# Kernel optimization log

Hardware: AMD Instinct MI355X
Metric: run time of the kernel (lower is better)

The kernel has to match this reference:

```python
import jax, jax.numpy as jnp
import numpy as np

N = 100000   # nodes
E = 1600000  # edges (before self-loops)
IN = 128     # in_num
H1, C1 = 8, 8    # gat1: 8 heads x 8 channels -> 64 concat
OUT = 32     # out_num (gat2: 1 head x 32)


def setup_inputs() -> dict:
    key = jax.random.key(0)
    ks = jax.random.split(key, 10)
    g = lambda k, shape, fan: (jax.random.normal(k, shape, jnp.float32) / np.sqrt(fan).astype(np.float32))
    return {
        "x": jax.random.normal(ks[0], (N, IN), jnp.float32),
        "edge_index": jax.random.randint(ks[1], (2, E), 0, N, dtype=jnp.int64),
        "W1": g(ks[2], (IN, H1 * C1), IN),
        "a_src1": g(ks[3], (H1, C1), C1),
        "a_dst1": g(ks[4], (H1, C1), C1),
        "b1": jnp.zeros((H1 * C1,), jnp.float32),
        "W2": g(ks[5], (H1 * C1, OUT), H1 * C1),
        "a_src2": g(ks[6], (1, OUT), OUT),
        "a_dst2": g(ks[7], (1, OUT), OUT),
        "b2": jnp.zeros((OUT,), jnp.float32),
    }


def _gat_layer(x, src, dst, W, a_src, a_dst, b, heads, ch):
    # PyG GATConv (concat=True, negative_slope=0.2). Dropout (p=0.6) is a
    # no-op in eval mode and omitted.
    n = x.shape[0]
    h = (x @ W).reshape(n, heads, ch)                        # [N,H,C]
    al_s = jnp.einsum('nhc,hc->nh', h, a_src)                # [N,H]
    al_d = jnp.einsum('nhc,hc->nh', h, a_dst)
    e = jax.nn.leaky_relu(al_s[src] + al_d[dst], negative_slope=0.2)  # [E,H]
    # segment softmax over incoming edges of each dst node
    m = jax.lax.stop_gradient(jax.ops.segment_max(e, dst, num_segments=n))
    ex = jnp.exp(e - m[dst])
    denom = jax.ops.segment_sum(ex, dst, num_segments=n)
    alpha = ex / denom[dst]                                  # [E,H]
    out = jax.ops.segment_sum(h[src] * alpha[:, :, None], dst, num_segments=n)
    return out.reshape(n, heads * ch) + b


def reference(x, edge_index, W1, a_src1, a_dst1, b1, W2, a_src2, a_dst2, b2):
    loop = jnp.arange(N, dtype=edge_index.dtype)
    src = jnp.concatenate([edge_index[0], loop])  # add_self_loops=True (PyG default)
    dst = jnp.concatenate([edge_index[1], loop])
    h = _gat_layer(x, src, dst, W1, a_src1, a_dst1, b1, H1, C1)   # [N,64]
    out = _gat_layer(h, src, dst, W2, a_src2, a_dst2, b2, 1, OUT)  # [N,OUT]
    return out
```

## Files before the change

### kernel.cpp

```cpp
#include <hip/hip_runtime.h>
#include <hip/hip_bf16.h>


#define SLAB  4096
#define NBUCK 512

typedef float v2f __attribute__((ext_vector_type(2)));

__device__ __forceinline__ float lrelu02(float x) { return x > 0.f ? x : 0.2f * x; }

__device__ __forceinline__ unsigned short f2bf(float v) {
    __hip_bfloat16 b = __float2bfloat16(v);
    return __builtin_bit_cast(unsigned short, b);
}

__device__ __forceinline__ void accum8(uint4 hv, float ex, v2f* acc) {
    v2f ex2 = {ex, ex};
#pragma unroll
    for (int q = 0; q < 4; ++q) {
        unsigned u = (&hv.x)[q];
        v2f h2 = {__uint_as_float(u << 16), __uint_as_float(u & 0xffff0000u)};
        acc[q] = __builtin_elementwise_fma(h2, ex2, acc[q]);
    }
}

__device__ __forceinline__ v2f shfl_xor_v2(v2f v, int mask) {
    v2f r;
    r.x = __shfl_xor(v.x, mask, 64);
    r.y = __shfl_xor(v.y, mask, 64);
    return r;
}

__device__ __forceinline__ void scatter_body(char* smem, int vbid,
                                             const int* __restrict__ ei,
                                             int e_real, int e_total, unsigned M,
                                             int* __restrict__ bcur_pad,
                                             int2* __restrict__ pairs) {
    int*  cnt   = (int*)smem;
    int*  loff  = cnt + 512;
    int*  lcur  = loff + 512;
    int*  gbase = lcur + 512;
    int*  ssrc  = gbase + 512;
    int*  sdst  = ssrc + 2048;
    unsigned short* bb = (unsigned short*)(sdst + 2048);

    const int t = threadIdx.x;
    const int base = vbid * 2048;
    cnt[t] = 0; cnt[t + 256] = 0;
    __syncthreads();

    int rs[8], rd[8], rb[8];
#pragma unroll
    for (int k = 0; k < 8; ++k) {
        int i = base + k * 256 + t;
        bool val = i < e_total;
        int s = 0, d = 0;
        if (val) {
            if (i < e_real) { s = ei[i]; d = ei[e_real + i]; }
            else            { s = d = i - e_real; }
        }
        int b = val ? (int)__umulhi((unsigned)d, M) : -1;
        rs[k] = s; rd[k] = d; rb[k] = b;
        if (val) atomicAdd(&cnt[b], 1);
    }
    __syncthreads();

    loff[t] = cnt[t]; loff[t + 256] = cnt[t + 256];
    __syncthreads();
    for (int off = 1; off < 512; off <<= 1) {
        int v0 = (t >= off) ? loff[t - off] : 0;
        int v1 = (t + 256 >= off) ? loff[t + 256 - off] : 0;
        __syncthreads();
        loff[t] += v0; loff[t + 256] += v1;
        __syncthreads();
    }
    int e0 = loff[t] - cnt[t];
    int e1 = loff[t + 256] - cnt[t + 256];
    loff[t] = e0;           loff[t + 256] = e1;
    lcur[t] = e0;           lcur[t + 256] = e1;
    gbase[t]       = t * SLAB         + atomicAdd(&bcur_pad[t * 16], cnt[t]);
    gbase[t + 256] = (t + 256) * SLAB + atomicAdd(&bcur_pad[(t + 256) * 16],
                                                  cnt[t + 256]);
    __syncthreads();

#pragma unroll
    for (int k = 0; k < 8; ++k) {
        if (rb[k] >= 0) {
            int lp = atomicAdd(&lcur[rb[k]], 1);
            ssrc[lp] = rs[k];
            sdst[lp] = rd[k];
            bb[lp]   = (unsigned short)rb[k];
        }
    }
    __syncthreads();

    int cn = e_total - base; if (cn > 2048) cn = 2048;
    for (int idx = t; idx < cn; idx += 256) {
        int b = bb[idx];
        int g = gbase[b] + (idx - loff[b]);
        pairs[g] = make_int2(ssrc[idx], sdst[idx]);
    }
}

template<int K, int OUTC, int H, int C, int NPT, int KCHUNK>
__device__ __forceinline__ void gemm_al_body(char* smem, int vbid,
                                             const float* __restrict__ x,
                                             const float* __restrict__ W,
                                             const float* __restrict__ a_src,
                                             const float* __restrict__ a_dst,
                                             unsigned short* __restrict__ h,
                                             float* __restrict__ al_s,
                                             float* __restrict__ al_d,
                                             int n) {
    constexpr int COLG = OUTC / 4;
    constexpr int NG   = 256 / COLG;
    static_assert(NG * 8 == NPT, "tile mismatch");
    constexpr int LDX  = KCHUNK + 1;
    float* Xs = (float*)smem;
    float* Ws = Xs + NPT * LDX;

    const int t    = threadIdx.x;
    const int mg   = t / COLG;
    const int cg   = t % COLG;
    const int base = vbid * NPT;

    float acc[8][4];
#pragma unroll
    for (int i = 0; i < 8; ++i)
#pragma unroll
        for (int j = 0; j < 4; ++j) acc[i][j] = 0.f;

    for (int kc = 0; kc < K; kc += KCHUNK) {
        __syncthreads();
        constexpr int F4R = KCHUNK / 4;
        constexpr int TOTF4 = NPT * F4R;
#pragma unroll
        for (int r = 0; r < TOTF4 / 256; ++r) {
            int f4   = r * 256 + t;
            int node = f4 / F4R;
            int kq   = f4 % F4R;
            int gn   = base + node; if (gn > n - 1) gn = n - 1;
            const float4 v = *(const float4*)&x[(size_t)gn * K + kc + kq * 4];
            float* d = &Xs[node * LDX + kq * 4];
            d[0] = v.x; d[1] = v.y; d[2] = v.z; d[3] = v.w;
        }
        constexpr int WF4 = KCHUNK * OUTC / 4;
        for (int idx = t; idx < WF4; idx += 256)
            *(float4*)&Ws[idx * 4] = *(const float4*)&W[(size_t)kc * OUTC + idx * 4];
        __syncthreads();

#pragma unroll 4
        for (int k = 0; k < KCHUNK; ++k) {
            float4 b = *(const float4*)&Ws[k * OUTC + cg * 4];
            float a[8];
#pragma unroll
            for (int i = 0; i < 8; ++i) a[i] = Xs[(mg * 8 + i) * LDX + k];
#pragma unroll
            for (int i = 0; i < 8; ++i) {
                acc[i][0] += a[i] * b.x;
                acc[i][1] += a[i] * b.y;
                acc[i][2] += a[i] * b.z;
                acc[i][3] += a[i] * b.w;
            }
        }
    }

    const float4 as4 = *(const float4*)&a_src[cg * 4];
    const float4 ad4 = *(const float4*)&a_dst[cg * 4];
    constexpr int GPH = C / 4;
    const int head = cg / GPH;
#pragma unroll
    for (int i = 0; i < 8; ++i) {
        int gn = base + mg * 8 + i;
        bool ok = gn < n;
        if (ok) {
            ushort4 hv;
            hv.x = f2bf(acc[i][0]); hv.y = f2bf(acc[i][1]);
            hv.z = f2bf(acc[i][2]); hv.w = f2bf(acc[i][3]);
            *(ushort4*)&h[(size_t)gn * OUTC + cg * 4] = hv;
        }
        float ps = acc[i][0] * as4.x + acc[i][1] * as4.y +
                   acc[i][2] * as4.z + acc[i][3] * as4.w;
        float pd = acc[i][0] * ad4.x + acc[i][1] * ad4.y +
                   acc[i][2] * ad4.z + acc[i][3] * ad4.w;
#pragma unroll
        for (int s = 1; s < GPH; s <<= 1) {
            ps += __shfl_xor(ps, s, 64);
            pd += __shfl_xor(pd, s, 64);
        }
        if (ok && (cg % GPH) == 0) {
            al_s[(size_t)gn * H + head] = ps;
            al_d[(size_t)gn * H + head] = pd;
        }
    }
}

__global__ __launch_bounds__(256)
void scatter_gemm_kernel(const int* __restrict__ ei, int e_real, int e_total,
                         unsigned M, int* __restrict__ bcur_pad,
                         int2* __restrict__ pairs, int ns,
                         const float* __restrict__ x,
                         const float* __restrict__ W1,
                         const float* __restrict__ as1,
                         const float* __restrict__ ad1,
                         unsigned short* __restrict__ h,
                         float* __restrict__ al_s,
                         float* __restrict__ al_d, int n) {
    __shared__ __align__(16) char smem[28672];
    if ((int)blockIdx.x < ns)
        scatter_body(smem, blockIdx.x, ei, e_real, e_total, M, bcur_pad, pairs);
    else
        gemm_al_body<128, 64, 8, 8, 128, 32>(smem, blockIdx.x - ns,
                                             x, W1, as1, ad1, h, al_s, al_d, n);
}

__global__ __launch_bounds__(256)
void csr_finalize_kernel(const int2* __restrict__ pairs,
                         const int* __restrict__ bcur_pad,
                         unsigned M, int n,
                         int* __restrict__ offsets,
                         int* __restrict__ srcs) {
    const int b = blockIdx.x;
    const int t = threadIdx.x;
    const unsigned long long Mll = M;
    int lo = (int)((((unsigned long long)b << 32) + Mll - 1) / Mll);
    int hi = (int)((((unsigned long long)(b + 1) << 32) + Mll - 1) / Mll);
    if (lo > n) lo = n;
    if (hi > n) hi = n;
    const int R    = hi - lo;
    const int cntb = bcur_pad[b * 16];
    const int2* sp = pairs + (size_t)b * SLAB;

    __shared__ int bs[NBUCK];
    __shared__ int ebeg_s;
    bs[t] = bcur_pad[t * 16];
    bs[t + 256] = bcur_pad[(t + 256) * 16];
    __syncthreads();
    for (int off = 1; off < NBUCK; off <<= 1) {
        int v0 = (t >= off) ? bs[t - off] : 0;
        int v1 = (t + 256 >= off) ? bs[t + 256 - off] : 0;
        __syncthreads();
        bs[t] += v0; bs[t + 256] += v1;
        __syncthreads();
    }
    if (t == 0) ebeg_s = (b == 0) ? 0 : bs[b - 1];
    if (b == NBUCK - 1 && t == 0) offsets[n] = bs[NBUCK - 1];
    __syncthreads();
    const int ebeg = ebeg_s;

    __shared__ int deg[256], sc[256], cur[256];
    deg[t] = 0;
    __syncthreads();
    for (int j = t; j < cntb; j += 256)
        atomicAdd(&deg[sp[j].y - lo], 1);
    __syncthreads();

    sc[t] = deg[t];
    __syncthreads();
    for (int off = 1; off < 256; off <<= 1) {
        int v = (t >= off) ? sc[t - off] : 0;
        __syncthreads();
        sc[t] += v;
        __syncthreads();
    }
    int e0 = sc[t] - deg[t];
    cur[t] = e0;
    if (t < R) offsets[lo + t] = ebeg + e0;
    __syncthreads();

    for (int j = t; j < cntb; j += 256) {
        int2 p = sp[j];
        int pos = atomicAdd(&cur[p.y - lo], 1);
        srcs[ebeg + pos] = p.x;
    }
}

__global__ __launch_bounds__(256)
void agg_gemm2_kernel(const int* __restrict__ offsets,
                      const int* __restrict__ srcs,
                      const float* __restrict__ al_s,
                      const float* __restrict__ al_d,
                      const unsigned short* __restrict__ hfeat,
                      const float* __restrict__ b1,
                      const float* __restrict__ W2,
                      const float* __restrict__ as2,
                      const float* __restrict__ ad2,
                      unsigned short* __restrict__ h2,
                      float* __restrict__ als2,
                      float* __restrict__ ald2, int n) {
    constexpr int H = 8, OUTC = 64, CG = 8, ES = 8;
    __shared__ float W2t[32 * 65];
    __shared__ float rowbuf[4][64];
    __shared__ float b1s[64], as2s[32], ad2s[32];

    const int t = threadIdx.x;
    for (int idx = t; idx < 2048; idx += 256) {
        int k = idx >> 5, j = idx & 31;
        W2t[j * 65 + k] = W2[idx];
    }
    if (t < 64)       b1s[t] = b1[t];
    else if (t < 96)  as2s[t - 64] = as2[t - 64];
    else if (t < 128) ad2s[t - 96] = ad2[t - 96];
    __syncthreads();

    const int wid0 = (int)((blockIdx.x * blockDim.x + t) >> 6);
    const int wid  = wid0 < n ? wid0 : n - 1;
    const int lane = t & 63;
    const int cg   = lane % CG;
    const int es   = lane / CG;
    const int head = cg;

    const float aldv = al_d[(size_t)wid * H + head];
    const int beg = offsets[wid];
    const int end = offsets[wid + 1];
    const int deg = end - beg;

    v2f acc[4];
#pragma unroll
    for (int q = 0; q < 4; ++q) acc[q] = (v2f){0.f, 0.f};
    float dsum = 0.f;

    if (deg <= ES) {
        int j = beg + es;
        bool v = j < end;
        int s = __builtin_nontemporal_load(&srcs[v ? j : beg]);
        const uint4 hv = *(const uint4*)&hfeat[(size_t)s * OUTC + cg * 8];
        float ls = al_s[(size_t)s * H + head];
        float ex = v ? __expf(lrelu02(ls + aldv)) : 0.f;
        accum8(hv, ex, acc);
        dsum += ex;
    } else if (deg <= 2 * ES) {
        int sA = __builtin_nontemporal_load(&srcs[beg + es]);
        int jB = beg + ES + es;
        bool vB = jB < end;
        int sB = __builtin_nontemporal_load(&srcs[vB ? jB : beg]);
        const uint4 hvA = *(const uint4*)&hfeat[(size_t)sA * OUTC + cg * 8];
        const uint4 hvB = *(const uint4*)&hfeat[(size_t)sB * OUTC + cg * 8];
        float lsA = al_s[(size_t)sA * H + head];
        float lsB = al_s[(size_t)sB * H + head];
        float exA = __expf(lrelu02(lsA + aldv));
        float exB = vB ? __expf(lrelu02(lsB + aldv)) : 0.f;
        accum8(hvA, exA, acc);
        accum8(hvB, exB, acc);
        dsum += exA + exB;
    } else if (deg <= 4 * ES) {
        int sA = __builtin_nontemporal_load(&srcs[beg + es]);
        int sB = __builtin_nontemporal_load(&srcs[beg + ES + es]);
        int jC = beg + 2 * ES + es;
        int jD = beg + 3 * ES + es;
        bool vC = jC < end;
        bool vD = jD < end;
        int sC = __builtin_nontemporal_load(&srcs[vC ? jC : beg]);
        int sD = __builtin_nontemporal_load(&srcs[vD ? jD : beg]);
        const uint4 hvA = *(const uint4*)&hfeat[(size_t)sA * OUTC + cg * 8];
        const uint4 hvB = *(const uint4*)&hfeat[(size_t)sB * OUTC + cg * 8];
        const uint4 hvC = *(const uint4*)&hfeat[(size_t)sC * OUTC + cg * 8];
        const uint4 hvD = *(const uint4*)&hfeat[(size_t)sD * OUTC + cg * 8];
        float lsA = al_s[(size_t)sA * H + head];
        float lsB = al_s[(size_t)sB * H + head];
        float lsC = al_s[(size_t)sC * H + head];
        float lsD = al_s[(size_t)sD * H + head];
        float exA = __expf(lrelu02(lsA + aldv));
        float exB = __expf(lrelu02(lsB + aldv));
        float exC = vC ? __expf(lrelu02(lsC + aldv)) : 0.f;
        float exD = vD ? __expf(lrelu02(lsD + aldv)) : 0.f;
        accum8(hvA, exA, acc);
        accum8(hvB, exB, acc);
        accum8(hvC, exC, acc);
        accum8(hvD, exD, acc);
        dsum += (exA + exB) + (exC + exD);
    } else {
        for (int j0 = beg; j0 < end; j0 += 2 * ES) {
            int jA = j0 + es;
            int jB = j0 + ES + es;
            bool vA = jA < end;
            bool vB = jB < end;
            int sA = __builtin_nontemporal_load(&srcs[vA ? jA : beg]);
            int sB = __builtin_nontemporal_load(&srcs[vB ? jB : beg]);
            const uint4 hvA = *(const uint4*)&hfeat[(size_t)sA * OUTC + cg * 8];
            const uint4 hvB = *(const uint4*)&hfeat[(size_t)sB * OUTC + cg * 8];
            float lsA = al_s[(size_t)sA * H + head];
            float lsB = al_s[(size_t)sB * H + head];
            float exA = vA ? __expf(lrelu02(lsA + aldv)) : 0.f;
            float exB = vB ? __expf(lrelu02(lsB + aldv)) : 0.f;
            accum8(hvA, exA, acc);
            accum8(hvB, exB, acc);
            dsum += exA + exB;
        }
    }

#pragma unroll
    for (int sh = CG; sh < 64; sh <<= 1) {
        dsum += __shfl_xor(dsum, sh, 64);
#pragma unroll
        for (int q = 0; q < 4; ++q) acc[q] += shfl_xor_v2(acc[q], sh);
    }

    const int w = t >> 6;
    if (es == 0) {
        float inv = 1.f / dsum;
#pragma unroll
        for (int q = 0; q < 4; ++q) {
            rowbuf[w][cg * 8 + 2 * q]     = acc[q].x * inv + b1s[cg * 8 + 2 * q];
            rowbuf[w][cg * 8 + 2 * q + 1] = acc[q].y * inv + b1s[cg * 8 + 2 * q + 1];
        }
    }
    __syncthreads();

    const int j  = lane & 31;
    const int kh = (lane >> 5) * 32;
    float o = 0.f;
#pragma unroll
    for (int it = 0; it < 8; ++it) {
        const float4 r = *(const float4*)&rowbuf[w][kh + it * 4];
        const float* wp = &W2t[j * 65 + kh + it * 4];
        o += r.x * wp[0] + r.y * wp[1] + r.z * wp[2] + r.w * wp[3];
    }
    o += __shfl_xor(o, 32, 64);

    float ps = o * as2s[j];
    float pd = o * ad2s[j];
#pragma unroll
    for (int s = 1; s < 32; s <<= 1) {
        ps += __shfl_xor(ps, s, 64);
        pd += __shfl_xor(pd, s, 64);
    }
    if (wid0 < n) {
        if (lane < 32) h2[(size_t)wid * 32 + j] = f2bf(o);
        if (lane == 0) { als2[wid] = ps; ald2[wid] = pd; }
    }
}

template<int H, int C>
__global__ __launch_bounds__(256)
void gat_agg_kernel(const int* __restrict__ offsets,
                    const int* __restrict__ srcs,
                    const float* __restrict__ al_s,
                    const float* __restrict__ al_d,
                    const unsigned short* __restrict__ hfeat,
                    const float* __restrict__ bias,
                    float* __restrict__ out, int n) {
    constexpr int OUTC = H * C;
    constexpr int CG   = OUTC / 8;
    constexpr int ES   = 64 / CG;
    const int wid  = (int)((blockIdx.x * blockDim.x + threadIdx.x) >> 6);
    const int lane = threadIdx.x & 63;
    const int cg   = lane % CG;
    const int es   = lane / CG;
    if (wid >= n) return;
    const int head = (cg * 8) / C;

    const float aldv = al_d[(size_t)wid * H + head];
    const int beg = offsets[wid];
    const int end = offsets[wid + 1];
    const int deg = end - beg;

    v2f acc[4];
#pragma unroll
    for (int q = 0; q < 4; ++q) acc[q] = (v2f){0.f, 0.f};
    float dsum = 0.f;

    if (deg <= ES) {
        int j = beg + es;
        bool v = j < end;
        int s = __builtin_nontemporal_load(&srcs[v ? j : beg]);
        const uint4 hv = *(const uint4*)&hfeat[(size_t)s * OUTC + cg * 8];
        float ls = al_s[(size_t)s * H + head];
        float ex = v ? __expf(lrelu02(ls + aldv)) : 0.f;
        accum8(hv, ex, acc);
        dsum += ex;
    } else if (deg <= 2 * ES) {
        int sA = __builtin_nontemporal_load(&srcs[beg + es]);
        int jB = beg + ES + es;
        bool vB = jB < end;
        int sB = __builtin_nontemporal_load(&srcs[vB ? jB : beg]);
        const uint4 hvA = *(const uint4*)&hfeat[(size_t)sA * OUTC + cg * 8];
        const uint4 hvB = *(const uint4*)&hfeat[(size_t)sB * OUTC + cg * 8];
        float lsA = al_s[(size_t)sA * H + head];
        float lsB = al_s[(size_t)sB * H + head];
        float exA = __expf(lrelu02(lsA + aldv));
        float exB = vB ? __expf(lrelu02(lsB + aldv)) : 0.f;
        accum8(hvA, exA, acc);
        accum8(hvB, exB, acc);
        dsum += exA + exB;
    } else if (deg <= 4 * ES) {
        int sA = __builtin_nontemporal_load(&srcs[beg + es]);
        int sB = __builtin_nontemporal_load(&srcs[beg + ES + es]);
        int jC = beg + 2 * ES + es;
        int jD = beg + 3 * ES + es;
        bool vC = jC < end;
        bool vD = jD < end;
        int sC = __builtin_nontemporal_load(&srcs[vC ? jC : beg]);
        int sD = __builtin_nontemporal_load(&srcs[vD ? jD : beg]);
        const uint4 hvA = *(const uint4*)&hfeat[(size_t)sA * OUTC + cg * 8];
        const uint4 hvB = *(const uint4*)&hfeat[(size_t)sB * OUTC + cg * 8];
        const uint4 hvC = *(const uint4*)&hfeat[(size_t)sC * OUTC + cg * 8];
        const uint4 hvD = *(const uint4*)&hfeat[(size_t)sD * OUTC + cg * 8];
        float lsA = al_s[(size_t)sA * H + head];
        float lsB = al_s[(size_t)sB * H + head];
        float lsC = al_s[(size_t)sC * H + head];
        float lsD = al_s[(size_t)sD * H + head];
        float exA = __expf(lrelu02(lsA + aldv));
        float exB = __expf(lrelu02(lsB + aldv));
        float exC = vC ? __expf(lrelu02(lsC + aldv)) : 0.f;
        float exD = vD ? __expf(lrelu02(lsD + aldv)) : 0.f;
        accum8(hvA, exA, acc);
        accum8(hvB, exB, acc);
        accum8(hvC, exC, acc);
        accum8(hvD, exD, acc);
        dsum += (exA + exB) + (exC + exD);
    } else {
        for (int j0 = beg; j0 < end; j0 += 2 * ES) {
            int jA = j0 + es;
            int jB = j0 + ES + es;
            bool vA = jA < end;
            bool vB = jB < end;
            int sA = __builtin_nontemporal_load(&srcs[vA ? jA : beg]);
            int sB = __builtin_nontemporal_load(&srcs[vB ? jB : beg]);
            const uint4 hvA = *(const uint4*)&hfeat[(size_t)sA * OUTC + cg * 8];
            const uint4 hvB = *(const uint4*)&hfeat[(size_t)sB * OUTC + cg * 8];
            float lsA = al_s[(size_t)sA * H + head];
            float lsB = al_s[(size_t)sB * H + head];
            float exA = vA ? __expf(lrelu02(lsA + aldv)) : 0.f;
            float exB = vB ? __expf(lrelu02(lsB + aldv)) : 0.f;
            accum8(hvA, exA, acc);
            accum8(hvB, exB, acc);
            dsum += exA + exB;
        }
    }

#pragma unroll
    for (int sh = CG; sh < 64; sh <<= 1) {
        dsum += __shfl_xor(dsum, sh, 64);
#pragma unroll
        for (int q = 0; q < 4; ++q) acc[q] += shfl_xor_v2(acc[q], sh);
    }

    if (es == 0) {
        float inv = 1.f / dsum;
        const float4 b0 = *(const float4*)&bias[cg * 8];
        const float4 b1v = *(const float4*)&bias[cg * 8 + 4];
        float4 o0, o1;
        o0.x = acc[0].x * inv + b0.x;
        o0.y = acc[0].y * inv + b0.y;
        o0.z = acc[1].x * inv + b0.z;
        o0.w = acc[1].y * inv + b0.w;
        o1.x = acc[2].x * inv + b1v.x;
        o1.y = acc[2].y * inv + b1v.y;
        o1.z = acc[3].x * inv + b1v.z;
        o1.w = acc[3].y * inv + b1v.w;
        *(float4*)&out[(size_t)wid * OUTC + cg * 8]     = o0;
        *(float4*)&out[(size_t)wid * OUTC + cg * 8 + 4] = o1;
    }
}


extern "C" void kernel_launch(void* const* d_in, const int* in_sizes, int n_in,
                              void* d_out, int out_size, void* d_ws, size_t ws_size,
                              hipStream_t stream) {
    const float* x   = (const float*)d_in[0];
    const int*   ei  = (const int*)  d_in[1];
    const float* W1  = (const float*)d_in[2];
    const float* as1 = (const float*)d_in[3];
    const float* ad1 = (const float*)d_in[4];
    const float* b1  = (const float*)d_in[5];
    const float* W2  = (const float*)d_in[6];
    const float* as2 = (const float*)d_in[7];
    const float* ad2 = (const float*)d_in[8];
    const float* b2  = (const float*)d_in[9];
    float* out = (float*)d_out;

    const int n       = in_sizes[0] / 128;
    const int e_real  = in_sizes[1] / 2;
    const int e_total = e_real + n;
    const unsigned M512 = (unsigned)(((unsigned long long)NBUCK << 32) / (unsigned)n);

    unsigned short* h1u = (unsigned short*)d_ws;
    float* fws  = (float*)d_ws;
    float* als1 = fws  + (size_t)n * 32;
    float* ald1 = als1 + (size_t)n * 8;
    float* scratch = ald1 + (size_t)n * 8;
    int2*  pairs = (int2*)scratch;
    unsigned short* h2 = (unsigned short*)scratch;
    float* als2 = scratch + (size_t)n * 16;
    float* ald2 = als2 + n;
    int* offsets  = (int*)(scratch + (size_t)n * 64);
    int* srcs     = offsets + (n + 1);
    int* bcur_pad = srcs + e_total;

    const int ns = (e_total + 2047) / 2048;
    const int g1 = (n + 127) / 128;

    hipMemsetAsync(bcur_pad, 0, NBUCK * 16 * sizeof(int), stream);
    scatter_gemm_kernel<<<ns + g1, 256, 0, stream>>>(
        ei, e_real, e_total, M512, bcur_pad, pairs, ns,
        x, W1, as1, ad1, h1u, als1, ald1, n);
    csr_finalize_kernel<<<NBUCK, 256, 0, stream>>>(pairs, bcur_pad, M512, n,
                                                   offsets, srcs);

    agg_gemm2_kernel<<<(n + 3) / 4, 256, 0, stream>>>(
        offsets, srcs, als1, ald1, h1u, b1, W2, as2, ad2, h2, als2, ald2, n);

    gat_agg_kernel<1, 32><<<(n + 3) / 4, 256, 0, stream>>>(
        offsets, srcs, als2, ald2, h2, b2, out, n);
}
```

Measured before the change: 310.9 us.

## Compute fused layer-2 GEMM from registers instead of shared memory staging

Drops the per-block shared-memory copy of W2, the bias and attention vectors, and the row buffer, along with both __syncthreads. Each lane instead loads an 8x4 slice of W2 into registers and computes partial 32-wide projections directly from its post-reduction accumulators, then combines them with cross-lane shuffles. This removes LDS setup and barriers, and lets out-of-range waves exit early. In exchange it adds about 40 registers per lane and repeats the W2 global loads in every wave, served from cache.

```diff
diff --git a/kernel.cpp b/kernel.cpp
--- a/kernel.cpp
+++ b/kernel.cpp
@@ -289,26 +289,22 @@
                       float* __restrict__ als2,
                       float* __restrict__ ald2, int n) {
     constexpr int H = 8, OUTC = 64, CG = 8, ES = 8;
-    __shared__ float W2t[32 * 65];
-    __shared__ float rowbuf[4][64];
-    __shared__ float b1s[64], as2s[32], ad2s[32];
-
-    const int t = threadIdx.x;
-    for (int idx = t; idx < 2048; idx += 256) {
-        int k = idx >> 5, j = idx & 31;
-        W2t[j * 65 + k] = W2[idx];
-    }
-    if (t < 64)       b1s[t] = b1[t];
-    else if (t < 96)  as2s[t - 64] = as2[t - 64];
-    else if (t < 128) ad2s[t - 96] = ad2[t - 96];
-    __syncthreads();
-
-    const int wid0 = (int)((blockIdx.x * blockDim.x + t) >> 6);
-    const int wid  = wid0 < n ? wid0 : n - 1;
+    const int t    = threadIdx.x;
+    const int wid  = (int)((blockIdx.x * blockDim.x + t) >> 6);
+    if (wid >= n) return;
     const int lane = t & 63;
     const int cg   = lane % CG;
     const int es   = lane / CG;
     const int head = cg;
+
+    float4 wreg[8];
+#pragma unroll
+    for (int k = 0; k < 8; ++k)
+        wreg[k] = *(const float4*)&W2[(size_t)(cg * 8 + k) * 32 + es * 4];
+    const float4 b1a = *(const float4*)&b1[cg * 8];
+    const float4 b1b = *(const float4*)&b1[cg * 8 + 4];
+    const float4 a2s = *(const float4*)&as2[es * 4];
+    const float4 a2d = *(const float4*)&ad2[es * 4];
 
     const float aldv = al_d[(size_t)wid * H + head];
     const int beg = offsets[wid];
@@ -396,39 +392,42 @@
         for (int q = 0; q < 4; ++q) acc[q] += shfl_xor_v2(acc[q], sh);
     }
 
-    const int w = t >> 6;
-    if (es == 0) {
-        float inv = 1.f / dsum;
-#pragma unroll
-        for (int q = 0; q < 4; ++q) {
-            rowbuf[w][cg * 8 + 2 * q]     = acc[q].x * inv + b1s[cg * 8 + 2 * q];
-            rowbuf[w][cg * 8 + 2 * q + 1] = acc[q].y * inv + b1s[cg * 8 + 2 * q + 1];
-        }
-    }
-    __syncthreads();
-
-    const int j  = lane & 31;
-    const int kh = (lane >> 5) * 32;
-    float o = 0.f;
-#pragma unroll
-    for (int it = 0; it < 8; ++it) {
-        const float4 r = *(const float4*)&rowbuf[w][kh + it * 4];
-        const float* wp = &W2t[j * 65 + kh + it * 4];
-        o += r.x * wp[0] + r.y * wp[1] + r.z * wp[2] + r.w * wp[3];
-    }
-    o += __shfl_xor(o, 32, 64);
-
-    float ps = o * as2s[j];
-    float pd = o * ad2s[j];
-#pragma unroll
-    for (int s = 1; s < 32; s <<= 1) {
+    const float inv = 1.f / dsum;
+    float r[8];
+    r[0] = acc[0].x * inv + b1a.x;  r[1] = acc[0].y * inv + b1a.y;
+    r[2] = acc[1].x * inv + b1a.z;  r[3] = acc[1].y * inv + b1a.w;
+    r[4] = acc[2].x * inv + b1b.x;  r[5] = acc[2].y * inv + b1b.y;
+    r[6] = acc[3].x * inv + b1b.z;  r[7] = acc[3].y * inv + b1b.w;
+
+    float p[4] = {0.f, 0.f, 0.f, 0.f};
+#pragma unroll
+    for (int k = 0; k < 8; ++k) {
+        p[0] += r[k] * wreg[k].x;
+        p[1] += r[k] * wreg[k].y;
+        p[2] += r[k] * wreg[k].z;
+        p[3] += r[k] * wreg[k].w;
+    }
+#pragma unroll
+    for (int s = 1; s < 8; s <<= 1) {
+#pragma unroll
+        for (int c = 0; c < 4; ++c) p[c] += __shfl_xor(p[c], s, 64);
+    }
+
+    if (cg == 0) {
+        ushort4 hv;
+        hv.x = f2bf(p[0]); hv.y = f2bf(p[1]);
+        hv.z = f2bf(p[2]); hv.w = f2bf(p[3]);
+        *(ushort4*)&h2[(size_t)wid * 32 + es * 4] = hv;
+    }
+
+    float ps = p[0] * a2s.x + p[1] * a2s.y + p[2] * a2s.z + p[3] * a2s.w;
+    float pd = p[0] * a2d.x + p[1] * a2d.y + p[2] * a2d.z + p[3] * a2d.w;
+#pragma unroll
+    for (int s = 8; s < 64; s <<= 1) {
         ps += __shfl_xor(ps, s, 64);
         pd += __shfl_xor(pd, s, 64);
     }
-    if (wid0 < n) {
-        if (lane < 32) h2[(size_t)wid * 32 + j] = f2bf(o);
-        if (lane == 0) { als2[wid] = ps; ald2[wid] = pd; }
-    }
+    if (lane == 0) { als2[wid] = ps; ald2[wid] = pd; }
 }
 
 template<int H, int C>
```

New measurement: 350.5 us. 1.13x slower.
